# Kernel tuning notes

Hardware: AMD Instinct MI355X
Metric: run time of the kernel (lower is better)

## Reference

```python
import jax, jax.numpy as jnp
import numpy as np

V, H, T, B = 32000, 1024, 512, 64

def setup_inputs() -> dict:
    key = jax.random.key(0)
    ks = jax.random.split(key, 20)
    tokens = jax.random.randint(ks[0], (T, B), 0, V)
    s_emb = 1.0 / np.sqrt(V)
    s_g = 1.0 / np.sqrt(2 * H)
    d = {
        'tokens': tokens,
        'emb_w': jax.random.uniform(ks[1], (H, V), jnp.float32, -s_emb, s_emb),
        'emb_b': jax.random.uniform(ks[2], (H,), jnp.float32, -s_emb, s_emb),
    }
    i = 3
    for pfx in ('fwd', 'bwd'):
        for g in ('i', 'o', 'f', 'g'):
            d[f'{pfx}_w{g}'] = jax.random.uniform(ks[i], (H, 2 * H), jnp.float32, -s_g, s_g); i += 1
            d[f'{pfx}_b{g}'] = jax.random.uniform(ks[i % 20], (H,), jnp.float32, -s_g, s_g)
    return d

def _run_lstm(xs, wi, bi, wo, bo, wf, bf, wg, bg):
    # xs: [T, B, H]; manual LSTM recurrence via lax.scan
    h0 = jnp.zeros((xs.shape[1], H), xs.dtype)
    c0 = jnp.zeros((xs.shape[1], H), xs.dtype)
    def step(carry, x):
        h, c = carry
        comb = jnp.concatenate([x, h], axis=1)          # [B, 2H]
        ig = jax.nn.sigmoid(comb @ wi.T + bi)
        og = jax.nn.sigmoid(comb @ wo.T + bo)
        fg = jax.nn.sigmoid(comb @ wf.T + bf)
        cg = jnp.tanh(comb @ wg.T + bg)
        c = fg * c + ig * cg
        h = og * jnp.tanh(c)
        return (h, c), (h, c)
    _, (hs, cs) = jax.lax.scan(step, (h0, c0), xs)
    return hs, cs                                       # [T, B, H] each

def reference(tokens, emb_w, emb_b,
              fwd_wi, fwd_bi, fwd_wo, fwd_bo, fwd_wf, fwd_bf, fwd_wg, fwd_bg,
              bwd_wi, bwd_bi, bwd_wo, bwd_bo, bwd_wf, bwd_bf, bwd_wg, bwd_bg):
    # one_hot(tokens) @ emb_w.T + emb_b == emb_w.T[tokens] + emb_b (dropout in eval mode)
    emb = emb_w.T[tokens] + emb_b                        # [T, B, H]
    f_hs, f_cs = _run_lstm(emb, fwd_wi, fwd_bi, fwd_wo, fwd_bo, fwd_wf, fwd_bf, fwd_wg, fwd_bg)
    # backward pass over reversed sequence; outputs kept in reversed-scan order,
    # matching the original's un-realigned list concatenation.
    b_hs, b_cs = _run_lstm(emb[::-1], bwd_wi, bwd_bi, bwd_wo, bwd_bo, bwd_wf, bwd_bf, bwd_wg, bwd_bg)
    hidden_states = jnp.concatenate([f_hs, b_hs], axis=2)   # [T, B, 2H]
    cell_states = jnp.concatenate([f_cs, b_cs], axis=2)     # [T, B, 2H]
    return hidden_states, cell_states
```

## Files before the change

### kernel.cpp

```cpp
#include <hip/hip_runtime.h>
#include <cstdint>
#include <cstddef>

#define V_SZ 32000
#define H_SZ 1024
#define T_SZ 512
#define B_SZ 64

typedef short short8 __attribute__((ext_vector_type(8)));
typedef float f32x4 __attribute__((ext_vector_type(4)));
typedef unsigned long long u64;

__device__ __forceinline__ short f2bf(float f) {
  union { float f; unsigned u; } v; v.f = f;
  unsigned r = (v.u + 0x7fffu + ((v.u >> 16) & 1u)) >> 16;
  return (short)r;
}

__device__ __forceinline__ void cs8(u64* p, u64 v) {
  __hip_atomic_store(p, v, __ATOMIC_RELAXED, __HIP_MEMORY_SCOPE_AGENT);
}

__global__ __launch_bounds__(256) void k_embT(const float* __restrict__ emb_w,
                                              const float* __restrict__ emb_b,
                                              short* __restrict__ embT) {
  __shared__ float tile[64][65];
  const int v0 = blockIdx.x * 64, h0 = blockIdx.y * 64;
  const int c = threadIdx.x & 63, rg = threadIdx.x >> 6;
#pragma unroll
  for (int p = 0; p < 16; ++p) {
    int r = rg * 16 + p;
    tile[r][c] = emb_w[(size_t)(h0 + r) * V_SZ + v0 + c];
  }
  __syncthreads();
  const float bias = emb_b[h0 + c];
#pragma unroll
  for (int p = 0; p < 16; ++p) {
    int vr = rg * 16 + p;
    embT[(size_t)(v0 + vr) * H_SZ + h0 + c] = f2bf(tile[c][vr] + bias);
  }
}

__global__ __launch_bounds__(256) void k_cast(const float* __restrict__ s,
                                              short* __restrict__ d, int n) {
  for (int i = blockIdx.x * 256 + threadIdx.x; i < n; i += gridDim.x * 256)
    d[i] = f2bf(s[i]);
}

__global__ __launch_bounds__(256) void k_copy(const float* __restrict__ s,
                                              float* __restrict__ d, int n) {
  for (int i = blockIdx.x * 256 + threadIdx.x; i < n; i += gridDim.x * 256)
    d[i] = s[i];
}

__global__ __launch_bounds__(512, 2) void k_persist(
    const int* __restrict__ tokens, const short* __restrict__ embT,
    const short* __restrict__ Wbf, const float* __restrict__ biasws,
    short* __restrict__ hbf, unsigned* __restrict__ bar,
    float* __restrict__ out) {
  __shared__ float P_lds[8][32][68];
  __shared__ short h_sh[32][16];

  const int tid = threadIdx.x;
  const int lane = tid & 63, w = tid >> 6;
  const int l15 = lane & 15, l4 = lane >> 4;
  const int d = (int)(blockIdx.x >> 7);
  const int bflat = (int)(blockIdx.x & 127);
  const int bg = bflat >> 6;
  const int cg = bflat & 63;
  const int n0 = cg << 4;
  const int r0 = bg * 32 + l15, r1 = r0 + 16;
  const int kw = w * 32 + l4 * 8;

  short8 Bf[8][4];
#pragma unroll
  for (int jj = 0; jj < 8; ++jj) {
    int slab = w + jj * 8;
#pragma unroll
    for (int nt = 0; nt < 4; ++nt) {
      int row64 = nt * 16 + l15;
      size_t grow = (size_t)((d * 4 + (row64 >> 4)) * 1024 + n0 + (row64 & 15));
      Bf[jj][nt] = *(const short8*)(Wbf + grow * 2048 + slab * 32 + l4 * 8);
    }
  }

  const int b32 = tid >> 4, c16 = tid & 15;
  const int gcol = n0 + c16, gbrow = bg * 32 + b32;
  float brg[4];
#pragma unroll
  for (int g4 = 0; g4 < 4; ++g4) brg[g4] = biasws[d * 4096 + g4 * 1024 + gcol];
  float c_reg = 0.f;

  const int grp = bflat >> 4;
  unsigned* const grpc = bar + 32 + (d * 8 + grp) * 16;
  unsigned* const root = bar + d * 16;

  const f32x4 fzero = {0.f, 0.f, 0.f, 0.f};
  f32x4 acc[2][4];

  auto X_PHASE = [&](int s) {
    const int td = d ? (T_SZ - 1 - s) : s;
    const short* xb0 = embT + (size_t)tokens[td * B_SZ + r0] * 1024 + kw;
    const short* xb1 = embT + (size_t)tokens[td * B_SZ + r1] * 1024 + kw;
    short8 xf[2][4];
#pragma unroll
    for (int jj = 0; jj < 4; ++jj) {
      xf[0][jj] = *(const short8*)(xb0 + jj * 256);
      xf[1][jj] = *(const short8*)(xb1 + jj * 256);
    }
#pragma unroll
    for (int ms = 0; ms < 2; ++ms)
#pragma unroll
      for (int nt = 0; nt < 4; ++nt) acc[ms][nt] = fzero;
#pragma unroll
    for (int jj = 0; jj < 4; ++jj)
#pragma unroll
      for (int ms = 0; ms < 2; ++ms)
#pragma unroll
        for (int nt = 0; nt < 4; ++nt)
          acc[ms][nt] = __builtin_amdgcn_mfma_f32_16x16x32_bf16(
              xf[ms][jj], Bf[jj][nt], acc[ms][nt], 0, 0, 0);
  };

  X_PHASE(0);

  for (int t = 0; t < T_SZ; ++t) {
    const short* hsrc = hbf + ((t & 1) * 2 + d) * 65536;
    short* hdst = hbf + (((t + 1) & 1) * 2 + d) * 65536;

    short8 hf[2][4];
    {
      const short* hb0 = hsrc + r0 * 1024 + kw;
      const short* hb1 = hsrc + r1 * 1024 + kw;
      asm volatile(
          "global_load_dwordx4 %0, %8, off sc0 sc1\n\t"
          "global_load_dwordx4 %1, %8, off offset:512 sc0 sc1\n\t"
          "global_load_dwordx4 %2, %8, off offset:1024 sc0 sc1\n\t"
          "global_load_dwordx4 %3, %8, off offset:1536 sc0 sc1\n\t"
          "global_load_dwordx4 %4, %9, off sc0 sc1\n\t"
          "global_load_dwordx4 %5, %9, off offset:512 sc0 sc1\n\t"
          "global_load_dwordx4 %6, %9, off offset:1024 sc0 sc1\n\t"
          "global_load_dwordx4 %7, %9, off offset:1536 sc0 sc1\n\t"
          "s_waitcnt vmcnt(0)"
          : "=&v"(hf[0][0]), "=&v"(hf[0][1]), "=&v"(hf[0][2]), "=&v"(hf[0][3]),
            "=&v"(hf[1][0]), "=&v"(hf[1][1]), "=&v"(hf[1][2]), "=&v"(hf[1][3])
          : "v"(hb0), "v"(hb1)
          : "memory");
    }
#pragma unroll
    for (int jj = 0; jj < 4; ++jj)
#pragma unroll
      for (int ms = 0; ms < 2; ++ms)
#pragma unroll
        for (int nt = 0; nt < 4; ++nt)
          acc[ms][nt] = __builtin_amdgcn_mfma_f32_16x16x32_bf16(
              hf[ms][jj], Bf[4 + jj][nt], acc[ms][nt], 0, 0, 0);

#pragma unroll
    for (int ms = 0; ms < 2; ++ms)
#pragma unroll
      for (int nt = 0; nt < 4; ++nt)
#pragma unroll
        for (int i = 0; i < 4; ++i)
          P_lds[w][ms * 16 + l4 * 4 + i][nt * 16 + l15] = acc[ms][nt][i];
    __syncthreads();

    float pr[4];
#pragma unroll
    for (int g4 = 0; g4 < 4; ++g4) {
      float s = brg[g4];
#pragma unroll
      for (int q = 0; q < 8; ++q) s += P_lds[q][b32][g4 * 16 + c16];
      pr[g4] = s;
    }
    float ig = 1.0f / (1.0f + expf(-pr[0]));
    float og = 1.0f / (1.0f + expf(-pr[1]));
    float fg = 1.0f / (1.0f + expf(-pr[2]));
    float cg4 = tanhf(pr[3]);
    c_reg = fg * c_reg + ig * cg4;
    float hnew = og * tanhf(c_reg);

    size_t o = (size_t)(t * B_SZ + gbrow) * 2048 + (size_t)d * 1024 + gcol;
    out[o] = hnew;
    out[o + 67108864] = c_reg;

    if (t < T_SZ - 1) {
      h_sh[b32][c16] = f2bf(hnew);
      __syncthreads();
      if (tid < 128) {
        int r = tid >> 2, qq = tid & 3;
        cs8((u64*)(hdst + (bg * 32 + r) * 1024 + n0 + qq * 4),
            *(const u64*)&h_sh[r][qq * 4]);
      }
      __syncthreads();
      if (tid == 0) {
        unsigned old = __hip_atomic_fetch_add(grpc, 1u, __ATOMIC_RELAXED,
                                              __HIP_MEMORY_SCOPE_AGENT);
        if (old == (unsigned)((t + 1) * 16 - 1))
          __hip_atomic_fetch_add(root, 1u, __ATOMIC_RELAXED,
                                 __HIP_MEMORY_SCOPE_AGENT);
      }
      X_PHASE(t + 1);
      if (tid == 0) {
        const unsigned tgt = (unsigned)((t + 1) * 8);
        while (__hip_atomic_load(root, __ATOMIC_RELAXED,
                                 __HIP_MEMORY_SCOPE_AGENT) < tgt)
          __builtin_amdgcn_s_sleep(2);
      }
      __syncthreads();
    }
  }
}

extern "C" void kernel_launch(void* const* d_in, const int* in_sizes, int n_in,
                              void* d_out, int out_size, void* d_ws, size_t ws_size,
                              hipStream_t stream) {
  (void)in_sizes; (void)n_in; (void)out_size; (void)ws_size;
  const int* tokens  = (const int*)d_in[0];
  const float* emb_w = (const float*)d_in[1];
  const float* emb_b = (const float*)d_in[2];

  char* ws = (char*)d_ws;
  short* embT   = (short*)(ws);
  short* Wbf    = (short*)(ws + 65536000);
  float* biasws = (float*)(ws + 99090432);
  short* hbf    = (short*)(ws + 99123200);
  unsigned* bar = (unsigned*)(ws + 99647488);

  (void)hipMemsetAsync(ws + 99123200, 0, 524288 + 2048, stream);

  k_embT<<<dim3(500, 16), 256, 0, stream>>>(emb_w, emb_b, embT);

  for (int d = 0; d < 2; ++d)
    for (int g = 0; g < 4; ++g) {
      const float* wsrc = (const float*)d_in[3 + d * 8 + g * 2];
      const float* bsrc = (const float*)d_in[4 + d * 8 + g * 2];
      k_cast<<<1024, 256, 0, stream>>>(wsrc, Wbf + (size_t)(d * 4 + g) * 1024 * 2048,
                                       1024 * 2048);
      k_copy<<<4, 256, 0, stream>>>(bsrc, biasws + (d * 4 + g) * 1024, 1024);
    }

  float* outp = (float*)d_out;
  void* kargs[] = {(void*)&tokens, (void*)&embT, (void*)&Wbf, (void*)&biasws,
                   (void*)&hbf, (void*)&bar, (void*)&outp};
  (void)hipLaunchCooperativeKernel((const void*)k_persist, dim3(256), dim3(512), kargs,
                                   0, stream);
}
```

Before: 3.335 ms.

## Read recurrent h from output buffer, unify barrier, fast activations, remap blocks

Removes the separate bf16 h ping-pong buffer. Each step now reads the previous h in fp32 directly from the output tensor and converts it to bf16 with packed convert instructions, which drops an LDS staging pass and one __syncthreads per step. Both directions now share a single root barrier, with blocks interleaved across directions and batch groups. It also swaps expf/tanhf for exp2/rcp approximations and writes h with wider dwordx4 stores after a wave shuffle. The trade-off is extra fp32 read traffic per step, a larger barrier that couples the two directions, and slightly lower activation accuracy.

```diff
diff --git a/kernel.cpp b/kernel.cpp
--- a/kernel.cpp
+++ b/kernel.cpp
@@ -17,8 +17,17 @@
   return (short)r;
 }
 
-__device__ __forceinline__ void cs8(u64* p, u64 v) {
-  __hip_atomic_store(p, v, __ATOMIC_RELAXED, __HIP_MEMORY_SCOPE_AGENT);
+__device__ __forceinline__ unsigned cvtpk(float a, float b) {
+  unsigned r;
+  asm("v_cvt_pk_bf16_f32 %0, %1, %2" : "=v"(r) : "v"(a), "v"(b));
+  return r;
+}
+
+__device__ __forceinline__ float fsig(float x) {
+  return __builtin_amdgcn_rcpf(1.f + __builtin_amdgcn_exp2f(x * -1.44269504f));
+}
+__device__ __forceinline__ float ftanh(float x) {
+  return 1.f - 2.f * __builtin_amdgcn_rcpf(1.f + __builtin_amdgcn_exp2f(x * 2.88539008f));
 }
 
 __global__ __launch_bounds__(256) void k_embT(const float* __restrict__ emb_w,
@@ -56,21 +65,22 @@
 __global__ __launch_bounds__(512, 2) void k_persist(
     const int* __restrict__ tokens, const short* __restrict__ embT,
     const short* __restrict__ Wbf, const float* __restrict__ biasws,
-    short* __restrict__ hbf, unsigned* __restrict__ bar,
-    float* __restrict__ out) {
+    unsigned* __restrict__ bar, float* __restrict__ out) {
   __shared__ float P_lds[8][32][68];
-  __shared__ short h_sh[32][16];
 
   const int tid = threadIdx.x;
   const int lane = tid & 63, w = tid >> 6;
   const int l15 = lane & 15, l4 = lane >> 4;
-  const int d = (int)(blockIdx.x >> 7);
-  const int bflat = (int)(blockIdx.x & 127);
-  const int bg = bflat >> 6;
-  const int cg = bflat & 63;
+  const int bid = (int)blockIdx.x;
+  const int m8 = bid & 7;
+  const int d = m8 >> 2;
+  const int bg = (m8 >> 1) & 1;
+  const int cg = (m8 & 1) * 32 + (bid >> 3);
   const int n0 = cg << 4;
   const int r0 = bg * 32 + l15, r1 = r0 + 16;
   const int kw = w * 32 + l4 * 8;
+
+  __threadfence();
 
   short8 Bf[8][4];
 #pragma unroll
@@ -91,9 +101,8 @@
   for (int g4 = 0; g4 < 4; ++g4) brg[g4] = biasws[d * 4096 + g4 * 1024 + gcol];
   float c_reg = 0.f;
 
-  const int grp = bflat >> 4;
-  unsigned* const grpc = bar + 32 + (d * 8 + grp) * 16;
-  unsigned* const root = bar + d * 16;
+  unsigned* const grpc = bar + 16 + (bid >> 4) * 16;
+  unsigned* const root = bar;
 
   const f32x4 fzero = {0.f, 0.f, 0.f, 0.f};
   f32x4 acc[2][4];
@@ -125,36 +134,32 @@
   X_PHASE(0);
 
   for (int t = 0; t < T_SZ; ++t) {
-    const short* hsrc = hbf + ((t & 1) * 2 + d) * 65536;
-    short* hdst = hbf + (((t + 1) & 1) * 2 + d) * 65536;
-
-    short8 hf[2][4];
-    {
-      const short* hb0 = hsrc + r0 * 1024 + kw;
-      const short* hb1 = hsrc + r1 * 1024 + kw;
-      asm volatile(
-          "global_load_dwordx4 %0, %8, off sc0 sc1\n\t"
-          "global_load_dwordx4 %1, %8, off offset:512 sc0 sc1\n\t"
-          "global_load_dwordx4 %2, %8, off offset:1024 sc0 sc1\n\t"
-          "global_load_dwordx4 %3, %8, off offset:1536 sc0 sc1\n\t"
-          "global_load_dwordx4 %4, %9, off sc0 sc1\n\t"
-          "global_load_dwordx4 %5, %9, off offset:512 sc0 sc1\n\t"
-          "global_load_dwordx4 %6, %9, off offset:1024 sc0 sc1\n\t"
-          "global_load_dwordx4 %7, %9, off offset:1536 sc0 sc1\n\t"
-          "s_waitcnt vmcnt(0)"
-          : "=&v"(hf[0][0]), "=&v"(hf[0][1]), "=&v"(hf[0][2]), "=&v"(hf[0][3]),
-            "=&v"(hf[1][0]), "=&v"(hf[1][1]), "=&v"(hf[1][2]), "=&v"(hf[1][3])
-          : "v"(hb0), "v"(hb1)
-          : "memory");
-    }
-#pragma unroll
-    for (int jj = 0; jj < 4; ++jj)
-#pragma unroll
-      for (int ms = 0; ms < 2; ++ms)
-#pragma unroll
-        for (int nt = 0; nt < 4; ++nt)
-          acc[ms][nt] = __builtin_amdgcn_mfma_f32_16x16x32_bf16(
-              hf[ms][jj], Bf[4 + jj][nt], acc[ms][nt], 0, 0, 0);
+    if (t > 0) {
+      const float* hb0 = out + ((size_t)(t - 1) * B_SZ + r0) * 2048 + (size_t)d * 1024 + kw;
+      const float* hb1 = out + ((size_t)(t - 1) * B_SZ + r1) * 2048 + (size_t)d * 1024 + kw;
+      short8 hf[2][4];
+#pragma unroll
+      for (int q = 0; q < 4; ++q) {
+        f32x4 a0 = *(const f32x4*)(hb0 + q * 256);
+        f32x4 a1 = *(const f32x4*)(hb0 + q * 256 + 4);
+        f32x4 b0 = *(const f32x4*)(hb1 + q * 256);
+        f32x4 b1 = *(const f32x4*)(hb1 + q * 256 + 4);
+        union { unsigned u[4]; short8 s; } c0, c1;
+        c0.u[0] = cvtpk(a0[0], a0[1]); c0.u[1] = cvtpk(a0[2], a0[3]);
+        c0.u[2] = cvtpk(a1[0], a1[1]); c0.u[3] = cvtpk(a1[2], a1[3]);
+        c1.u[0] = cvtpk(b0[0], b0[1]); c1.u[1] = cvtpk(b0[2], b0[3]);
+        c1.u[2] = cvtpk(b1[0], b1[1]); c1.u[3] = cvtpk(b1[2], b1[3]);
+        hf[0][q] = c0.s; hf[1][q] = c1.s;
+      }
+#pragma unroll
+      for (int q = 0; q < 4; ++q)
+#pragma unroll
+        for (int ms = 0; ms < 2; ++ms)
+#pragma unroll
+          for (int nt = 0; nt < 4; ++nt)
+            acc[ms][nt] = __builtin_amdgcn_mfma_f32_16x16x32_bf16(
+                hf[ms][q], Bf[4 + q][nt], acc[ms][nt], 0, 0, 0);
+    }
 
 #pragma unroll
     for (int ms = 0; ms < 2; ++ms)
@@ -173,25 +178,27 @@
       for (int q = 0; q < 8; ++q) s += P_lds[q][b32][g4 * 16 + c16];
       pr[g4] = s;
     }
-    float ig = 1.0f / (1.0f + expf(-pr[0]));
-    float og = 1.0f / (1.0f + expf(-pr[1]));
-    float fg = 1.0f / (1.0f + expf(-pr[2]));
-    float cg4 = tanhf(pr[3]);
+    float ig = fsig(pr[0]);
+    float og = fsig(pr[1]);
+    float fg = fsig(pr[2]);
+    float cg4 = ftanh(pr[3]);
     c_reg = fg * c_reg + ig * cg4;
-    float hnew = og * tanhf(c_reg);
-
-    size_t o = (size_t)(t * B_SZ + gbrow) * 2048 + (size_t)d * 1024 + gcol;
-    out[o] = hnew;
-    out[o + 67108864] = c_reg;
+    float hnew = og * ftanh(c_reg);
+
+    {
+      float s1 = __shfl_down(hnew, 1);
+      float s2 = __shfl_down(hnew, 2);
+      float s3 = __shfl_down(hnew, 3);
+      if ((lane & 3) == 0) {
+        f32x4 pk = {hnew, s1, s2, s3};
+        float* p = out + ((size_t)t * B_SZ + bg * 32 + (w * 4 + (lane >> 4))) * 2048 +
+                   (size_t)d * 1024 + n0 + (lane & 15);
+        asm volatile("global_store_dwordx4 %0, %1, off sc0 sc1"
+                     :: "v"(p), "v"(pk) : "memory");
+      }
+    }
 
     if (t < T_SZ - 1) {
-      h_sh[b32][c16] = f2bf(hnew);
-      __syncthreads();
-      if (tid < 128) {
-        int r = tid >> 2, qq = tid & 3;
-        cs8((u64*)(hdst + (bg * 32 + r) * 1024 + n0 + qq * 4),
-            *(const u64*)&h_sh[r][qq * 4]);
-      }
       __syncthreads();
       if (tid == 0) {
         unsigned old = __hip_atomic_fetch_add(grpc, 1u, __ATOMIC_RELAXED,
@@ -200,14 +207,17 @@
           __hip_atomic_fetch_add(root, 1u, __ATOMIC_RELAXED,
                                  __HIP_MEMORY_SCOPE_AGENT);
       }
+      out[((size_t)t * B_SZ + gbrow) * 2048 + (size_t)d * 1024 + gcol + 67108864] = c_reg;
       X_PHASE(t + 1);
       if (tid == 0) {
-        const unsigned tgt = (unsigned)((t + 1) * 8);
+        const unsigned tgt = (unsigned)((t + 1) * 16);
         while (__hip_atomic_load(root, __ATOMIC_RELAXED,
                                  __HIP_MEMORY_SCOPE_AGENT) < tgt)
           __builtin_amdgcn_s_sleep(2);
       }
       __syncthreads();
+    } else {
+      out[((size_t)t * B_SZ + gbrow) * 2048 + (size_t)d * 1024 + gcol + 67108864] = c_reg;
     }
   }
 }
@@ -224,10 +234,9 @@
   short* embT   = (short*)(ws);
   short* Wbf    = (short*)(ws + 65536000);
   float* biasws = (float*)(ws + 99090432);
-  short* hbf    = (short*)(ws + 99123200);
-  unsigned* bar = (unsigned*)(ws + 99647488);
-
-  (void)hipMemsetAsync(ws + 99123200, 0, 524288 + 2048, stream);
+  unsigned* bar = (unsigned*)(ws + 99123200);
+
+  (void)hipMemsetAsync(ws + 99123200, 0, 2048, stream);
 
   k_embT<<<dim3(500, 16), 256, 0, stream>>>(emb_w, emb_b, embT);
 
@@ -242,7 +251,7 @@
 
   float* outp = (float*)d_out;
   void* kargs[] = {(void*)&tokens, (void*)&embT, (void*)&Wbf, (void*)&biasws,
-                   (void*)&hbf, (void*)&bar, (void*)&outp};
+                   (void*)&bar, (void*)&outp};
   (void)hipLaunchCooperativeKernel((const void*)k_persist, dim3(256), dim3(512), kargs,
                                    0, stream);
 }
```

Result: slower. 3.960 ms (+18.7%).

## Replace hierarchical counter barrier with per-block flag polling and fast activations

Applied to the files above, without the earlier changes.

The per-step grid barrier changes from a two-level atomic counter tree to per-block step flags. Each block stores its step number to its own flag, and a full wavefront polls the 64 flags of its batch group with a wave-wide all-check. This limits the dependency to the blocks that produce the needed h rows and removes a serialized atomic hop. Sigmoid and tanh now use the hardware exp2 and rcp intrinsics, the output stores move after the flag publish so they overlap the wait, step 0 skips the h GEMM, and the memset shrinks to cover only the flag area, so the h buffer is no longer zeroed.

```diff
diff --git a/kernel.cpp b/kernel.cpp
--- a/kernel.cpp
+++ b/kernel.cpp
@@ -19,6 +19,13 @@
 
 __device__ __forceinline__ void cs8(u64* p, u64 v) {
   __hip_atomic_store(p, v, __ATOMIC_RELAXED, __HIP_MEMORY_SCOPE_AGENT);
+}
+
+__device__ __forceinline__ float fsig(float x) {
+  return __builtin_amdgcn_rcpf(1.f + __builtin_amdgcn_exp2f(x * -1.44269504f));
+}
+__device__ __forceinline__ float ftanh(float x) {
+  return 1.f - 2.f * __builtin_amdgcn_rcpf(1.f + __builtin_amdgcn_exp2f(x * 2.88539008f));
 }
 
 __global__ __launch_bounds__(256) void k_embT(const float* __restrict__ emb_w,
@@ -91,9 +98,7 @@
   for (int g4 = 0; g4 < 4; ++g4) brg[g4] = biasws[d * 4096 + g4 * 1024 + gcol];
   float c_reg = 0.f;
 
-  const int grp = bflat >> 4;
-  unsigned* const grpc = bar + 32 + (d * 8 + grp) * 16;
-  unsigned* const root = bar + d * 16;
+  unsigned* const gflags = bar + (d * 2 + bg) * 64;
 
   const f32x4 fzero = {0.f, 0.f, 0.f, 0.f};
   f32x4 acc[2][4];
@@ -125,13 +130,11 @@
   X_PHASE(0);
 
   for (int t = 0; t < T_SZ; ++t) {
-    const short* hsrc = hbf + ((t & 1) * 2 + d) * 65536;
-    short* hdst = hbf + (((t + 1) & 1) * 2 + d) * 65536;
-
-    short8 hf[2][4];
-    {
+    if (t > 0) {
+      const short* hsrc = hbf + ((t & 1) * 2 + d) * 65536;
       const short* hb0 = hsrc + r0 * 1024 + kw;
       const short* hb1 = hsrc + r1 * 1024 + kw;
+      short8 hf[2][4];
       asm volatile(
           "global_load_dwordx4 %0, %8, off sc0 sc1\n\t"
           "global_load_dwordx4 %1, %8, off offset:512 sc0 sc1\n\t"
@@ -146,15 +149,15 @@
             "=&v"(hf[1][0]), "=&v"(hf[1][1]), "=&v"(hf[1][2]), "=&v"(hf[1][3])
           : "v"(hb0), "v"(hb1)
           : "memory");
-    }
-#pragma unroll
-    for (int jj = 0; jj < 4; ++jj)
-#pragma unroll
-      for (int ms = 0; ms < 2; ++ms)
-#pragma unroll
-        for (int nt = 0; nt < 4; ++nt)
-          acc[ms][nt] = __builtin_amdgcn_mfma_f32_16x16x32_bf16(
-              hf[ms][jj], Bf[4 + jj][nt], acc[ms][nt], 0, 0, 0);
+#pragma unroll
+      for (int q = 0; q < 4; ++q)
+#pragma unroll
+        for (int ms = 0; ms < 2; ++ms)
+#pragma unroll
+          for (int nt = 0; nt < 4; ++nt)
+            acc[ms][nt] = __builtin_amdgcn_mfma_f32_16x16x32_bf16(
+                hf[ms][q], Bf[4 + q][nt], acc[ms][nt], 0, 0, 0);
+    }
 
 #pragma unroll
     for (int ms = 0; ms < 2; ++ms)
@@ -173,18 +176,15 @@
       for (int q = 0; q < 8; ++q) s += P_lds[q][b32][g4 * 16 + c16];
       pr[g4] = s;
     }
-    float ig = 1.0f / (1.0f + expf(-pr[0]));
-    float og = 1.0f / (1.0f + expf(-pr[1]));
-    float fg = 1.0f / (1.0f + expf(-pr[2]));
-    float cg4 = tanhf(pr[3]);
+    float ig = fsig(pr[0]);
+    float og = fsig(pr[1]);
+    float fg = fsig(pr[2]);
+    float cg4 = ftanh(pr[3]);
     c_reg = fg * c_reg + ig * cg4;
-    float hnew = og * tanhf(c_reg);
-
-    size_t o = (size_t)(t * B_SZ + gbrow) * 2048 + (size_t)d * 1024 + gcol;
-    out[o] = hnew;
-    out[o + 67108864] = c_reg;
+    float hnew = og * ftanh(c_reg);
 
     if (t < T_SZ - 1) {
+      short* hdst = hbf + (((t + 1) & 1) * 2 + d) * 65536;
       h_sh[b32][c16] = f2bf(hnew);
       __syncthreads();
       if (tid < 128) {
@@ -193,21 +193,29 @@
             *(const u64*)&h_sh[r][qq * 4]);
       }
       __syncthreads();
-      if (tid == 0) {
-        unsigned old = __hip_atomic_fetch_add(grpc, 1u, __ATOMIC_RELAXED,
-                                              __HIP_MEMORY_SCOPE_AGENT);
-        if (old == (unsigned)((t + 1) * 16 - 1))
-          __hip_atomic_fetch_add(root, 1u, __ATOMIC_RELAXED,
-                                 __HIP_MEMORY_SCOPE_AGENT);
-      }
+      if (tid == 0)
+        __hip_atomic_store(gflags + cg, (unsigned)(t + 1), __ATOMIC_RELAXED,
+                           __HIP_MEMORY_SCOPE_AGENT);
+
+      size_t o = (size_t)(t * B_SZ + gbrow) * 2048 + (size_t)d * 1024 + gcol;
+      out[o] = hnew;
+      out[o + 67108864] = c_reg;
       X_PHASE(t + 1);
-      if (tid == 0) {
-        const unsigned tgt = (unsigned)((t + 1) * 8);
-        while (__hip_atomic_load(root, __ATOMIC_RELAXED,
-                                 __HIP_MEMORY_SCOPE_AGENT) < tgt)
-          __builtin_amdgcn_s_sleep(2);
+
+      if (w == 0) {
+        const unsigned tgt = (unsigned)(t + 1);
+        while (true) {
+          unsigned v = __hip_atomic_load(gflags + lane, __ATOMIC_RELAXED,
+                                         __HIP_MEMORY_SCOPE_AGENT);
+          if (__all(v >= tgt)) break;
+          __builtin_amdgcn_s_sleep(1);
+        }
       }
       __syncthreads();
+    } else {
+      size_t o = (size_t)(t * B_SZ + gbrow) * 2048 + (size_t)d * 1024 + gcol;
+      out[o] = hnew;
+      out[o + 67108864] = c_reg;
     }
   }
 }
@@ -227,7 +235,7 @@
   short* hbf    = (short*)(ws + 99123200);
   unsigned* bar = (unsigned*)(ws + 99647488);
 
-  (void)hipMemsetAsync(ws + 99123200, 0, 524288 + 2048, stream);
+  (void)hipMemsetAsync(ws + 99647488, 0, 1024, stream);
 
   k_embT<<<dim3(500, 16), 256, 0, stream>>>(emb_w, emb_b, embT);
 
```

Measured after the change: 3.101 ms. 7.0% less time.
